# Optimization experiments

Hardware: AMD Instinct MI355X
Metric: run time of the kernel (lower is better)

## Reference

```python
import jax, jax.numpy as jnp
import numpy as np

B, S, H = 2, 4096, 2048
NH, HD = 16, 128
BLOCK = 256
EPS = 1e-5


def setup_inputs() -> dict:
    key = jax.random.key(0)
    ks = jax.random.split(key, 6)
    return {
        "hidden_states": jax.random.normal(ks[0], (B, S, H), jnp.float32),
        "attention_mask": jnp.ones((B, S), jnp.float32),
        "slope_rate": jax.random.uniform(ks[1], (NH,), jnp.float32),
        "w_qkv": jax.random.normal(ks[2], (H, 3 * NH * HD), jnp.float32) * 0.02,
        "w_gate": jax.random.normal(ks[3], (H, NH * HD), jnp.float32) * 0.02,
        "w_out": jax.random.normal(ks[4], (NH * HD, H), jnp.float32) * 0.02,
        "norm_weight": jnp.ones((NH * HD,), jnp.float32),
    }


def _lightning_attention(q, k, v, slope):
    # q,k,v: [b,h,n,d]; slope: [h] positive decay rates
    b, h, n, d = q.shape
    nc = n // BLOCK
    ar = jnp.arange(BLOCK, dtype=q.dtype) + 1.0  # 1..BLOCK
    s = slope[:, None, None]  # [h,1,1]
    q_decay = jnp.exp(-s * ar[None, :, None])             # [h,BLOCK,1]
    k_decay = jnp.exp(-s * (BLOCK - ar)[None, :, None])   # [h,BLOCK,1]
    idx = ar[:, None] - ar[None, :]                        # [BLOCK,BLOCK]
    mask = (idx >= 0).astype(q.dtype)
    # mask idx before exp so masked entries don't overflow (keeps grads finite)
    diag_decay = jnp.exp(-s * (idx * mask)[None]) * mask[None]  # [h,BLOCK,BLOCK]
    block_decay = jnp.exp(-slope * BLOCK)[None, :, None, None]  # [1,h,1,1]

    def to_chunks(x):
        return x.reshape(b, h, nc, BLOCK, d).transpose(2, 0, 1, 3, 4)

    qc, kc, vc = to_chunks(q), to_chunks(k), to_chunks(v)

    def step(kv, xs):
        qi, ki, vi = xs  # [b,h,BLOCK,d]
        # inter-chunk: decayed query against carried state kv [b,h,d,d]
        o_inter = jnp.einsum("bhmd,bhde->bhme", qi * q_decay, kv)
        # intra-chunk: causal decayed attention
        attn = jnp.einsum("bhmd,bhnd->bhmn", qi, ki) * diag_decay
        o = o_inter + jnp.einsum("bhmn,bhne->bhme", attn, vi)
        kv = block_decay * kv + jnp.einsum("bhnd,bhne->bhde", ki * k_decay, vi)
        return kv, o

    kv0 = jnp.zeros((b, h, d, d), q.dtype)
    _, o = jax.lax.scan(step, kv0, (qc, kc, vc))  # o: [nc,b,h,BLOCK,d]
    return o.transpose(1, 2, 0, 3, 4).reshape(b, h, n, d)


def reference(hidden_states, attention_mask, slope_rate, w_qkv, w_gate, w_out, norm_weight):
    b, n, _ = hidden_states.shape
    qkv = jax.nn.silu(hidden_states @ w_qkv)  # act on fused qkv
    q, k, v = jnp.split(qkv, 3, axis=-1)

    def heads(x):
        return x.reshape(b, n, NH, HD).transpose(0, 2, 1, 3)

    q, k, v = heads(q), heads(k), heads(v)
    v = v * attention_mask[:, None, :, None]  # zero padded tokens
    o = _lightning_attention(q, k, v, slope_rate)  # [b,h,n,d]
    o = o.transpose(0, 2, 1, 3).reshape(b, n, NH * HD)
    # RMSNorm over head_dim*num_heads
    var = jnp.mean(o * o, axis=-1, keepdims=True)
    o = o * jax.lax.rsqrt(var + EPS) * norm_weight
    # sigmoid output gate from raw hidden_states
    o = jax.nn.sigmoid(hidden_states @ w_gate) * o
    return o @ w_out
```

## Files before the change

### kernel.cpp

```cpp
#include <hip/hip_runtime.h>
#include <cstdint>

#define B_ 2
#define S_ 4096
#define H_ 2048
#define NH_ 16
#define HD_ 128
#define BLOCK_ 256
#define NC_ (S_/BLOCK_)
#define M_ (B_*S_)
#define EPS_ 1e-5f

typedef unsigned short ushort_t;
typedef unsigned short u16x4 __attribute__((ext_vector_type(4)));
typedef short frag_ab __attribute__((ext_vector_type(8)));
typedef float frag_cd __attribute__((ext_vector_type(4)));

static __device__ inline float bf2f(ushort_t u) {
    union { unsigned int i; float f; } x;
    x.i = ((unsigned int)u) << 16;
    return x.f;
}
static __device__ inline ushort_t f2bf(float f) {
    union { float f; unsigned int i; } x;
    x.f = f;
    unsigned int r = x.i + 0x7fffu + ((x.i >> 16) & 1u);
    return (ushort_t)(r >> 16);
}

static __device__ __forceinline__ void gload_lds16(const ushort_t* g, ushort_t* l) {
    __builtin_amdgcn_global_load_lds(
        (__attribute__((address_space(1))) void*)(uintptr_t)g,
        (__attribute__((address_space(3))) void*)l,
        16, 0, 0);
}

__global__ __launch_bounds__(256)
void cast_bf16_kernel(const float* __restrict__ in, ushort_t* __restrict__ out)
{
    int i = blockIdx.x * 256 + threadIdx.x;
    float4 v = reinterpret_cast<const float4*>(in)[i];
    u16x4 o = { f2bf(v.x), f2bf(v.y), f2bf(v.z), f2bf(v.w) };
    *reinterpret_cast<u16x4*>(&out[(size_t)i * 4]) = o;
}

__global__ __launch_bounds__(256)
void transpose_cast_kernel(const float* __restrict__ W, ushort_t* __restrict__ WT,
                           int K, int N)
{
    __shared__ float t[32][33];
    const int kb = blockIdx.y * 32, nb = blockIdx.x * 32;
    const int tx = threadIdx.x & 31, ty = threadIdx.x >> 5;
    #pragma unroll
    for (int i = 0; i < 4; ++i)
        t[ty + i * 8][tx] = W[(size_t)(kb + ty + i * 8) * N + nb + tx];
    __syncthreads();
    #pragma unroll
    for (int i = 0; i < 4; ++i)
        WT[(size_t)(nb + ty + i * 8) * K + kb + tx] = f2bf(t[tx][ty + i * 8]);
}

template<int MODE>
__global__ __launch_bounds__(256)
void gemm_mfma(const ushort_t* __restrict__ A, const ushort_t* __restrict__ BT,
               int M, int N, int K,
               float* __restrict__ Cf, ushort_t* __restrict__ Cb,
               ushort_t* __restrict__ qo, ushort_t* __restrict__ ko,
               ushort_t* __restrict__ kTo, ushort_t* __restrict__ vTo,
               const float* __restrict__ mask)
{
    __shared__ __align__(16) ushort_t As[128 * 32];
    __shared__ __align__(16) ushort_t Bs[128 * 32];
    const int tid  = threadIdx.x;
    const int lane = tid & 63, wid = tid >> 6;
    const int wr = wid >> 1, wc = wid & 1;
    const int l15 = lane & 15, l4 = lane >> 4;
    const int rowBase = blockIdx.y * 128, colBase = blockIdx.x * 128;

    const int srow = tid >> 2;
    const int sk   = (tid & 3) * 8;

    frag_cd acc[4][4];
    #pragma unroll
    for (int m = 0; m < 4; ++m)
        #pragma unroll
        for (int n = 0; n < 4; ++n) acc[m][n] = 0.f;

    for (int kt = 0; kt < K; kt += 32) {
        __syncthreads();
        #pragma unroll
        for (int j = 0; j < 2; ++j) {
            gload_lds16(A  + (size_t)(rowBase + j * 64 + srow) * K + kt + sk,
                        &As[j * 2048 + wid * 512]);
            gload_lds16(BT + (size_t)(colBase + j * 64 + srow) * K + kt + sk,
                        &Bs[j * 2048 + wid * 512]);
        }
        __syncthreads();

        frag_ab af[4], bf[4];
        #pragma unroll
        for (int m = 0; m < 4; ++m)
            af[m] = *reinterpret_cast<const frag_ab*>(&As[(wr * 64 + m * 16 + l15) * 32 + l4 * 8]);
        #pragma unroll
        for (int n = 0; n < 4; ++n)
            bf[n] = *reinterpret_cast<const frag_ab*>(&Bs[(wc * 64 + n * 16 + l15) * 32 + l4 * 8]);
        #pragma unroll
        for (int m = 0; m < 4; ++m)
            #pragma unroll
            for (int n = 0; n < 4; ++n)
                acc[m][n] = __builtin_amdgcn_mfma_f32_16x16x32_bf16(af[m], bf[n], acc[m][n], 0, 0, 0);
    }

    const int orow0 = rowBase + wr * 64;
    const int ocol0 = colBase + wc * 64;
    if (MODE == 0) {
        #pragma unroll
        for (int m = 0; m < 4; ++m)
            #pragma unroll
            for (int n = 0; n < 4; ++n)
                #pragma unroll
                for (int r = 0; r < 4; ++r) {
                    int row = orow0 + m * 16 + l4 * 4 + r;
                    int col = ocol0 + n * 16 + l15;
                    Cf[(size_t)row * N + col] = acc[m][n][r];
                }
    } else if (MODE == 1) {
        #pragma unroll
        for (int m = 0; m < 4; ++m)
            #pragma unroll
            for (int n = 0; n < 4; ++n)
                #pragma unroll
                for (int r = 0; r < 4; ++r) {
                    int row = orow0 + m * 16 + l4 * 4 + r;
                    int col = ocol0 + n * 16 + l15;
                    float x = acc[m][n][r];
                    Cb[(size_t)row * N + col] = f2bf(1.f / (1.f + __expf(-x)));
                }
    } else {
        const int which = colBase >> 11;
        const int h     = (colBase >> 7) & 15;
        #pragma unroll
        for (int m = 0; m < 4; ++m) {
            int row0 = orow0 + m * 16 + l4 * 4;
            int b = row0 >> 12, sr0 = row0 & 4095;
            int bh = b * NH_ + h;
            #pragma unroll
            for (int n = 0; n < 4; ++n) {
                int d = (ocol0 & 127) + n * 16 + l15;
                float sv[4];
                #pragma unroll
                for (int r = 0; r < 4; ++r) {
                    float x = acc[m][n][r];
                    sv[r] = x / (1.f + __expf(-x));
                }
                if (which == 0) {
                    #pragma unroll
                    for (int r = 0; r < 4; ++r)
                        qo[((size_t)bh * S_ + sr0 + r) * HD_ + d] = f2bf(sv[r]);
                } else if (which == 1) {
                    u16x4 pk;
                    #pragma unroll
                    for (int r = 0; r < 4; ++r) {
                        ushort_t u = f2bf(sv[r]);
                        ko[((size_t)bh * S_ + sr0 + r) * HD_ + d] = u;
                        pk[r] = u;
                    }
                    *reinterpret_cast<u16x4*>(&kTo[((size_t)bh * HD_ + d) * S_ + sr0]) = pk;
                } else {
                    u16x4 pk;
                    #pragma unroll
                    for (int r = 0; r < 4; ++r)
                        pk[r] = f2bf(sv[r] * mask[b * S_ + sr0 + r]);
                    *reinterpret_cast<u16x4*>(&vTo[((size_t)bh * HD_ + d) * S_ + sr0]) = pk;
                }
            }
        }
    }
}

__global__ __launch_bounds__(256)
void kv_chunk_mfma(const ushort_t* __restrict__ kT, const ushort_t* __restrict__ vT,
                   const float* __restrict__ slope, ushort_t* __restrict__ kvT)
{
    const int c = blockIdx.x, bh = blockIdx.y;
    const float s = slope[bh & 15];
    const int tid = threadIdx.x, lane = tid & 63, w = tid >> 6;
    const int l15 = lane & 15, l4 = lane >> 4;
    __shared__ float dec[BLOCK_];
    __shared__ __align__(16) ushort_t VTl[128 * 64];
    __shared__ __align__(16) ushort_t KTl[128 * 64];
    dec[tid] = __expf(-s * (float)(BLOCK_ - 1 - tid));

    frag_cd acc[2][8];
    #pragma unroll
    for (int mf = 0; mf < 2; ++mf)
        #pragma unroll
        for (int df = 0; df < 8; ++df) acc[mf][df] = 0.f;

    for (int nt = 0; nt < 4; ++nt) {
        __syncthreads();
        #pragma unroll
        for (int i = 0; i < 4; ++i) {
            int u = tid + i * 256;
            int row = u >> 3, slot = u & 7;
            size_t gsrc = ((size_t)bh * HD_ + row) * S_ + c * BLOCK_ + nt * 64 + slot * 8;
            frag_ab v8 = *reinterpret_cast<const frag_ab*>(vT + gsrc);
            *reinterpret_cast<frag_ab*>((char*)VTl + row * 128 + ((slot * 16) ^ ((row & 7) << 4))) = v8;
            frag_ab k8 = *reinterpret_cast<const frag_ab*>(kT + gsrc);
            frag_ab kd;
            #pragma unroll
            for (int j = 0; j < 8; ++j)
                kd[j] = (short)f2bf(bf2f((ushort_t)k8[j]) * dec[nt * 64 + slot * 8 + j]);
            *reinterpret_cast<frag_ab*>((char*)KTl + row * 128 + ((slot * 16) ^ ((row & 7) << 4))) = kd;
        }
        __syncthreads();
        #pragma unroll
        for (int ks = 0; ks < 2; ++ks) {
            frag_ab a[2];
            #pragma unroll
            for (int mf = 0; mf < 2; ++mf)
                a[mf] = *reinterpret_cast<const frag_ab*>(
                    (char*)VTl + (w * 32 + mf * 16 + l15) * 128 + ((ks * 64 + l4 * 16) ^ ((l15 & 7) << 4)));
            #pragma unroll
            for (int df = 0; df < 8; ++df) {
                frag_ab bk = *reinterpret_cast<const frag_ab*>(
                    (char*)KTl + (df * 16 + l15) * 128 + ((ks * 64 + l4 * 16) ^ ((l15 & 7) << 4)));
                acc[0][df] = __builtin_amdgcn_mfma_f32_16x16x32_bf16(a[0], bk, acc[0][df], 0, 0, 0);
                acc[1][df] = __builtin_amdgcn_mfma_f32_16x16x32_bf16(a[1], bk, acc[1][df], 0, 0, 0);
            }
        }
    }
    ushort_t* out = kvT + ((size_t)bh * NC_ + c) * 16384;
    #pragma unroll
    for (int mf = 0; mf < 2; ++mf)
        #pragma unroll
        for (int df = 0; df < 8; ++df)
            #pragma unroll
            for (int r = 0; r < 4; ++r) {
                int e = w * 32 + mf * 16 + l4 * 4 + r;
                int d = df * 16 + l15;
                out[e * 128 + d] = f2bf(acc[mf][df][r]);
            }
}

__global__ __launch_bounds__(256)
void kv_scan_kernel(const float* __restrict__ slope, const ushort_t* __restrict__ kvT,
                    ushort_t* __restrict__ sT)
{
    const int es = blockIdx.x, bh = blockIdx.y;
    const float s = slope[bh & 15];
    const float bd = __expf(-s * (float)BLOCK_);
    const int tid = threadIdx.x;
    float st[16];
    #pragma unroll
    for (int i = 0; i < 16; ++i) st[i] = 0.f;
    for (int c = 0; c < NC_; ++c) {
        const ushort_t* p = kvT + ((size_t)bh * NC_ + c) * 16384;
        ushort_t* qp = sT + ((size_t)bh * NC_ + c) * 16384;
        #pragma unroll
        for (int i = 0; i < 16; ++i) {
            int lin = tid + i * 256;
            int off = (lin >> 5) * 128 + es * 32 + (lin & 31);
            float x = bf2f(p[off]);
            qp[off] = f2bf(st[i]);
            st[i] = bd * st[i] + x;
        }
    }
}

__global__ __launch_bounds__(512)
void attn_mfma(const ushort_t* __restrict__ q, const ushort_t* __restrict__ k,
               const ushort_t* __restrict__ vT, const ushort_t* __restrict__ sT,
               const float* __restrict__ slope, float* __restrict__ o)
{
    const int c = blockIdx.x, bh = blockIdx.y;
    const int h = bh & 15, b = bh >> 4;
    const float s = slope[h];
    const int tid = threadIdx.x, lane = tid & 63, w = tid >> 6;
    const int l15 = lane & 15, l4 = lane >> 4;

    __shared__ __align__(16) ushort_t SH[16384];
    __shared__ __align__(16) ushort_t P[8][2048];

    frag_ab aq[2][4];
    #pragma unroll
    for (int mf = 0; mf < 2; ++mf)
        #pragma unroll
        for (int ks = 0; ks < 4; ++ks) {
            int row = c * BLOCK_ + w * 32 + mf * 16 + l15;
            aq[mf][ks] = *reinterpret_cast<const frag_ab*>(
                q + ((size_t)bh * S_ + row) * HD_ + ks * 32 + l4 * 8);
        }

    frag_cd oa[2][8];
    #pragma unroll
    for (int mf = 0; mf < 2; ++mf)
        #pragma unroll
        for (int ef = 0; ef < 8; ++ef) oa[mf][ef] = 0.f;

    const int wrow = w * 32;
    for (int nt = 0; nt < 4; ++nt) {
        __syncthreads();
        #pragma unroll
        for (int i = 0; i < 2; ++i) {
            int u = tid + i * 512;
            int n = u >> 4, slot = u & 15;
            frag_ab k8 = *reinterpret_cast<const frag_ab*>(
                k + ((size_t)bh * S_ + c * BLOCK_ + nt * 64 + n) * HD_ + slot * 8);
            *reinterpret_cast<frag_ab*>((char*)SH + n * 256 + ((slot * 16) ^ ((n & 7) << 4))) = k8;
        }
        #pragma unroll
        for (int i = 0; i < 2; ++i) {
            int u = tid + i * 512;
            int e = u >> 3, slot = u & 7;
            frag_ab v8 = *reinterpret_cast<const frag_ab*>(
                vT + ((size_t)bh * HD_ + e) * S_ + c * BLOCK_ + nt * 64 + slot * 8);
            *reinterpret_cast<frag_ab*>((char*)SH + 16384 + e * 128 + ((slot * 16) ^ ((e & 7) << 4))) = v8;
        }
        __syncthreads();
        if (nt * 64 > wrow + 31) continue;

        frag_cd pacc[2][4];
        #pragma unroll
        for (int mf = 0; mf < 2; ++mf)
            #pragma unroll
            for (int nf = 0; nf < 4; ++nf) pacc[mf][nf] = 0.f;
        #pragma unroll
        for (int ks = 0; ks < 4; ++ks)
            #pragma unroll
            for (int nf = 0; nf < 4; ++nf) {
                frag_ab bk = *reinterpret_cast<const frag_ab*>(
                    (char*)SH + (nf * 16 + l15) * 256 + ((ks * 64 + l4 * 16) ^ ((l15 & 7) << 4)));
                pacc[0][nf] = __builtin_amdgcn_mfma_f32_16x16x32_bf16(aq[0][ks], bk, pacc[0][nf], 0, 0, 0);
                pacc[1][nf] = __builtin_amdgcn_mfma_f32_16x16x32_bf16(aq[1][ks], bk, pacc[1][nf], 0, 0, 0);
            }
        #pragma unroll
        for (int mf = 0; mf < 2; ++mf)
            #pragma unroll
            for (int nf = 0; nf < 4; ++nf)
                #pragma unroll
                for (int r = 0; r < 4; ++r) {
                    int m = mf * 16 + l4 * 4 + r;
                    int mrow = wrow + m;
                    int ncol = nt * 64 + nf * 16 + l15;
                    float pv = 0.f;
                    if (mrow >= ncol) pv = pacc[mf][nf][r] * __expf(s * (float)(ncol - mrow));
                    *reinterpret_cast<ushort_t*>(
                        (char*)&P[w][0] + m * 128 + (((nf * 16 + l15) * 2) ^ ((m & 7) << 4))) = f2bf(pv);
                }
        __builtin_amdgcn_sched_barrier(0);
        #pragma unroll
        for (int ks = 0; ks < 2; ++ks) {
            frag_ab ap[2];
            #pragma unroll
            for (int mf = 0; mf < 2; ++mf)
                ap[mf] = *reinterpret_cast<const frag_ab*>(
                    (char*)&P[w][0] + (mf * 16 + l15) * 128 + ((ks * 64 + l4 * 16) ^ ((l15 & 7) << 4)));
            #pragma unroll
            for (int ef = 0; ef < 8; ++ef) {
                frag_ab bv = *reinterpret_cast<const frag_ab*>(
                    (char*)SH + 16384 + (ef * 16 + l15) * 128 + ((ks * 64 + l4 * 16) ^ ((l15 & 7) << 4)));
                oa[0][ef] = __builtin_amdgcn_mfma_f32_16x16x32_bf16(ap[0], bv, oa[0][ef], 0, 0, 0);
                oa[1][ef] = __builtin_amdgcn_mfma_f32_16x16x32_bf16(ap[1], bv, oa[1][ef], 0, 0, 0);
            }
        }
    }

    __syncthreads();
    #pragma unroll
    for (int i = 0; i < 4; ++i) {
        int u = tid + i * 512;
        int e = u >> 4, slot = u & 15;
        frag_ab s8 = *reinterpret_cast<const frag_ab*>(
            sT + ((size_t)(bh * NC_ + c)) * 16384 + e * 128 + slot * 8);
        *reinterpret_cast<frag_ab*>((char*)SH + e * 256 + ((slot * 16) ^ ((e & 7) << 4))) = s8;
    }
    __syncthreads();
    #pragma unroll
    for (int mf = 0; mf < 2; ++mf) {
        float qd = __expf(-s * (float)(wrow + mf * 16 + l15 + 1));
        #pragma unroll
        for (int ks = 0; ks < 4; ++ks) {
            frag_ab v = aq[mf][ks];
            #pragma unroll
            for (int j = 0; j < 8; ++j)
                v[j] = (short)f2bf(bf2f((ushort_t)v[j]) * qd);
            aq[mf][ks] = v;
        }
    }
    #pragma unroll
    for (int ks = 0; ks < 4; ++ks)
        #pragma unroll
        for (int ef = 0; ef < 8; ++ef) {
            frag_ab bs = *reinterpret_cast<const frag_ab*>(
                (char*)SH + (ef * 16 + l15) * 256 + ((ks * 64 + l4 * 16) ^ ((l15 & 7) << 4)));
            oa[0][ef] = __builtin_amdgcn_mfma_f32_16x16x32_bf16(aq[0][ks], bs, oa[0][ef], 0, 0, 0);
            oa[1][ef] = __builtin_amdgcn_mfma_f32_16x16x32_bf16(aq[1][ks], bs, oa[1][ef], 0, 0, 0);
        }
    #pragma unroll
    for (int mf = 0; mf < 2; ++mf)
        #pragma unroll
        for (int ef = 0; ef < 8; ++ef)
            #pragma unroll
            for (int r = 0; r < 4; ++r) {
                int row = c * BLOCK_ + wrow + mf * 16 + l4 * 4 + r;
                int col = h * HD_ + ef * 16 + l15;
                o[((size_t)(b * S_ + row)) * H_ + col] = oa[mf][ef][r];
            }
}

__global__ __launch_bounds__(256)
void norm_gate_kernel(const float* __restrict__ o, const ushort_t* __restrict__ gate,
                      const float* __restrict__ nw, ushort_t* __restrict__ on)
{
    const int row = blockIdx.x;
    const int tid = threadIdx.x;
    const float* orow = o + (size_t)row * H_;
    const ushort_t* grow = gate + (size_t)row * H_;
    ushort_t* onrow = on + (size_t)row * H_;
    float vals[8];
    float ss = 0.f;
    #pragma unroll
    for (int i = 0; i < 8; ++i) {
        vals[i] = orow[tid + i * 256];
        ss += vals[i] * vals[i];
    }
    __shared__ float red[256];
    red[tid] = ss;
    __syncthreads();
    #pragma unroll
    for (int st = 128; st > 0; st >>= 1) {
        if (tid < st) red[tid] += red[tid + st];
        __syncthreads();
    }
    float scale = rsqrtf(red[0] * (1.f / (float)H_) + EPS_);
    #pragma unroll
    for (int i = 0; i < 8; ++i) {
        int cidx = tid + i * 256;
        onrow[cidx] = f2bf(vals[i] * scale * nw[cidx] * bf2f(grow[cidx]));
    }
}

extern "C" void kernel_launch(void* const* d_in, const int* in_sizes, int n_in,
                              void* d_out, int out_size, void* d_ws, size_t ws_size,
                              hipStream_t stream)
{
    const float* hidden = (const float*)d_in[0];
    const float* mask   = (const float*)d_in[1];
    const float* slope  = (const float*)d_in[2];
    const float* w_qkv  = (const float*)d_in[3];
    const float* w_gate = (const float*)d_in[4];
    const float* w_out  = (const float*)d_in[5];
    const float* nw     = (const float*)d_in[6];

    const size_t MH = (size_t)M_ * H_;
    ushort_t* hid_bf  = (ushort_t*)d_ws;
    ushort_t* on_ws   = hid_bf;
    ushort_t* wqkvT   = hid_bf + MH;
    ushort_t* wgateT  = wqkvT + (size_t)6144 * 2048;
    ushort_t* kvT_ws  = wqkvT;
    ushort_t* sT_ws   = wqkvT + MH / 2;
    ushort_t* woutT   = wqkvT;
    ushort_t* q_ws    = hid_bf + 2 * MH;
    ushort_t* k_ws    = q_ws + MH;
    ushort_t* vT_ws   = k_ws + MH;
    ushort_t* gate_ws = vT_ws + MH;
    ushort_t* kT_ws   = (ushort_t*)d_out;
    float*    o_f32   = (float*)d_out;

    dim3 blk(256);
    cast_bf16_kernel<<<(MH / 4) / 256, blk, 0, stream>>>(hidden, hid_bf);
    transpose_cast_kernel<<<dim3(6144 / 32, 2048 / 32), blk, 0, stream>>>(w_qkv, wqkvT, 2048, 6144);
    transpose_cast_kernel<<<dim3(2048 / 32, 2048 / 32), blk, 0, stream>>>(w_gate, wgateT, 2048, 2048);
    gemm_mfma<2><<<dim3(6144 / 128, M_ / 128), blk, 0, stream>>>(
        hid_bf, wqkvT, M_, 6144, 2048, nullptr, nullptr, q_ws, k_ws, kT_ws, vT_ws, mask);
    gemm_mfma<1><<<dim3(2048 / 128, M_ / 128), blk, 0, stream>>>(
        hid_bf, wgateT, M_, 2048, 2048, nullptr, gate_ws, nullptr, nullptr, nullptr, nullptr, nullptr);
    kv_chunk_mfma<<<dim3(NC_, B_ * NH_), blk, 0, stream>>>(kT_ws, vT_ws, slope, kvT_ws);
    kv_scan_kernel<<<dim3(4, B_ * NH_), blk, 0, stream>>>(slope, kvT_ws, sT_ws);
    attn_mfma<<<dim3(NC_, B_ * NH_), dim3(512), 0, stream>>>(
        q_ws, k_ws, vT_ws, sT_ws, slope, o_f32);
    transpose_cast_kernel<<<dim3(2048 / 32, 2048 / 32), blk, 0, stream>>>(w_out, woutT, 2048, 2048);
    norm_gate_kernel<<<M_, blk, 0, stream>>>(o_f32, gate_ws, nw, on_ws);
    gemm_mfma<0><<<dim3(2048 / 128, M_ / 128), blk, 0, stream>>>(
        on_ws, woutT, M_, 2048, 2048, (float*)d_out, nullptr, nullptr, nullptr, nullptr, nullptr, nullptr);
}
```

Before: 655.3 us.

## Replace GEMMs with 256x256 double-buffered swizzled MFMA kernel and fuse gate GEMM

Replaces the 128x128 single-buffered GEMM with a 256x256-tile, 512-thread kernel. It double-buffers LDS with XOR-swizzled layout, staggers global-to-LDS loads between MFMA phases with explicit waitcnt and barriers, raises wave priority during MFMA, and remaps workgroups for L2 locality. The gate projection is fused into the QKV GEMM by treating w_qkv and w_gate as one contiguous 8192-column weight, with a sigmoid epilogue on the last column range. This is meant to raise MFMA utilisation and cut one launch, but it relies on the weight workspaces being adjacent and on hand-tuned wait counts being correct.

```diff
diff --git a/kernel.cpp b/kernel.cpp
--- a/kernel.cpp
+++ b/kernel.cpp
@@ -35,6 +35,12 @@
         16, 0, 0);
 }
 
+#define FENCE_ asm volatile("" ::: "memory")
+#define LGKM0_ asm volatile("s_waitcnt lgkmcnt(0)" ::: "memory")
+#define VMW2_  asm volatile("s_waitcnt vmcnt(2)" ::: "memory")
+#define VMW4_  asm volatile("s_waitcnt vmcnt(4)" ::: "memory")
+#define VMW0_  asm volatile("s_waitcnt vmcnt(0)" ::: "memory")
+
 __global__ __launch_bounds__(256)
 void cast_bf16_kernel(const float* __restrict__ in, ushort_t* __restrict__ out)
 {
@@ -61,117 +67,211 @@
 }
 
 template<int MODE>
-__global__ __launch_bounds__(256)
-void gemm_mfma(const ushort_t* __restrict__ A, const ushort_t* __restrict__ BT,
-               int M, int N, int K,
-               float* __restrict__ Cf, ushort_t* __restrict__ Cb,
-               ushort_t* __restrict__ qo, ushort_t* __restrict__ ko,
-               ushort_t* __restrict__ kTo, ushort_t* __restrict__ vTo,
-               const float* __restrict__ mask)
-{
-    __shared__ __align__(16) ushort_t As[128 * 32];
-    __shared__ __align__(16) ushort_t Bs[128 * 32];
+__global__ __launch_bounds__(512, 2)
+void gemm256(const ushort_t* __restrict__ A, const ushort_t* __restrict__ BT,
+             int M, int N, int K,
+             float* __restrict__ Cf,
+             ushort_t* __restrict__ qo, ushort_t* __restrict__ ko,
+             ushort_t* __restrict__ kTo, ushort_t* __restrict__ vTo,
+             ushort_t* __restrict__ gateo, const float* __restrict__ mask)
+{
+    __shared__ __align__(16) ushort_t LA[2][16384];
+    __shared__ __align__(16) ushort_t LB[2][16384];
+
     const int tid  = threadIdx.x;
     const int lane = tid & 63, wid = tid >> 6;
-    const int wr = wid >> 1, wc = wid & 1;
+    const int wm = wid >> 2, wn = wid & 3;
     const int l15 = lane & 15, l4 = lane >> 4;
-    const int rowBase = blockIdx.y * 128, colBase = blockIdx.x * 128;
-
-    const int srow = tid >> 2;
-    const int sk   = (tid & 3) * 8;
-
-    frag_cd acc[4][4];
-    #pragma unroll
-    for (int m = 0; m < 4; ++m)
+    const int trow = tid >> 3;
+    const int xk   = (tid & 7) ^ (trow & 7);
+
+    const int nwg = gridDim.x;
+    const int lin = blockIdx.x;
+    const int virt = (lin & 7) * (nwg >> 3) + (lin >> 3);
+    const int NBX = N >> 8;
+    const int by = virt / NBX, bx = virt - by * NBX;
+    const int rowBase = by * 256, colBase = bx * 256;
+
+    frag_cd acc[8][4];
+    #pragma unroll
+    for (int m = 0; m < 8; ++m)
         #pragma unroll
         for (int n = 0; n < 4; ++n) acc[m][n] = 0.f;
 
-    for (int kt = 0; kt < K; kt += 32) {
-        __syncthreads();
-        #pragma unroll
-        for (int j = 0; j < 2; ++j) {
-            gload_lds16(A  + (size_t)(rowBase + j * 64 + srow) * K + kt + sk,
-                        &As[j * 2048 + wid * 512]);
-            gload_lds16(BT + (size_t)(colBase + j * 64 + srow) * K + kt + sk,
-                        &Bs[j * 2048 + wid * 512]);
-        }
-        __syncthreads();
-
-        frag_ab af[4], bf[4];
-        #pragma unroll
-        for (int m = 0; m < 4; ++m)
-            af[m] = *reinterpret_cast<const frag_ab*>(&As[(wr * 64 + m * 16 + l15) * 32 + l4 * 8]);
-        #pragma unroll
-        for (int n = 0; n < 4; ++n)
-            bf[n] = *reinterpret_cast<const frag_ab*>(&Bs[(wc * 64 + n * 16 + l15) * 32 + l4 * 8]);
-        #pragma unroll
-        for (int m = 0; m < 4; ++m)
-            #pragma unroll
-            for (int n = 0; n < 4; ++n)
-                acc[m][n] = __builtin_amdgcn_mfma_f32_16x16x32_bf16(af[m], bf[n], acc[m][n], 0, 0, 0);
-    }
-
-    const int orow0 = rowBase + wr * 64;
-    const int ocol0 = colBase + wc * 64;
+    frag_ab fa[4][2];
+    frag_ab fb[2][2][2];
+
+    #define RDF(Lp, row_, sl_) \
+        (*reinterpret_cast<const frag_ab*>( \
+            reinterpret_cast<const char*>(Lp) + (row_) * 128 + ((((sl_) ^ ((row_) & 7)) & 7) << 4)))
+    #define STG(Gp, base_, i_, kt_, Lp) \
+        gload_lds16((Gp) + (size_t)((base_) + (i_) * 64 + trow) * K + (kt_) + xk * 8, \
+                    (Lp) + (i_) * 4096 + wid * 512)
+
+    const int NT = K >> 6;
+    int cur = 0;
+    STG(BT, colBase, 0, 0, LB[0]); STG(BT, colBase, 1, 0, LB[0]);
+    STG(BT, colBase, 2, 0, LB[0]); STG(BT, colBase, 3, 0, LB[0]);
+    STG(A,  rowBase, 0, 0, LA[0]); STG(A,  rowBase, 2, 0, LA[0]);
+    STG(A,  rowBase, 1, 0, LA[0]); STG(A,  rowBase, 3, 0, LA[0]);
+    VMW2_; FENCE_; __builtin_amdgcn_s_barrier();
+
+    for (int t = 0; t < NT; ++t) {
+        const ushort_t* Ab = LA[cur];
+        const ushort_t* Bb = LB[cur];
+        ushort_t* An = LA[cur ^ 1];
+        ushort_t* Bn = LB[cur ^ 1];
+        const int ktn = (t + 1) << 6;
+        const bool more = (t + 1) < NT;
+
+        #pragma unroll
+        for (int mi = 0; mi < 4; ++mi)
+            #pragma unroll
+            for (int ks = 0; ks < 2; ++ks)
+                fa[mi][ks] = RDF(Ab, wm * 128 + mi * 16 + l15, ks * 4 + l4);
+        #pragma unroll
+        for (int ni = 0; ni < 2; ++ni)
+            #pragma unroll
+            for (int ks = 0; ks < 2; ++ks)
+                fb[0][ni][ks] = RDF(Bb, wn * 64 + ni * 16 + l15, ks * 4 + l4);
+        if (more) { STG(BT, colBase, 0, ktn, Bn); STG(BT, colBase, 1, ktn, Bn); }
+        FENCE_; __builtin_amdgcn_s_barrier(); LGKM0_;
+        __builtin_amdgcn_sched_barrier(0);
+        __builtin_amdgcn_s_setprio(1);
+        #pragma unroll
+        for (int mi = 0; mi < 4; ++mi)
+            #pragma unroll
+            for (int ni = 0; ni < 2; ++ni)
+                #pragma unroll
+                for (int ks = 0; ks < 2; ++ks)
+                    acc[mi][ni] = __builtin_amdgcn_mfma_f32_16x16x32_bf16(
+                        fa[mi][ks], fb[0][ni][ks], acc[mi][ni], 0, 0, 0);
+        __builtin_amdgcn_s_setprio(0);
+        FENCE_; __builtin_amdgcn_s_barrier();
+
+        #pragma unroll
+        for (int ni = 0; ni < 2; ++ni)
+            #pragma unroll
+            for (int ks = 0; ks < 2; ++ks)
+                fb[1][ni][ks] = RDF(Bb, wn * 64 + 32 + ni * 16 + l15, ks * 4 + l4);
+        if (more) { STG(BT, colBase, 2, ktn, Bn); STG(BT, colBase, 3, ktn, Bn); VMW4_; }
+        else      { VMW0_; }
+        FENCE_; __builtin_amdgcn_s_barrier(); LGKM0_;
+        __builtin_amdgcn_sched_barrier(0);
+        __builtin_amdgcn_s_setprio(1);
+        #pragma unroll
+        for (int mi = 0; mi < 4; ++mi)
+            #pragma unroll
+            for (int ni = 0; ni < 2; ++ni)
+                #pragma unroll
+                for (int ks = 0; ks < 2; ++ks)
+                    acc[mi][2 + ni] = __builtin_amdgcn_mfma_f32_16x16x32_bf16(
+                        fa[mi][ks], fb[1][ni][ks], acc[mi][2 + ni], 0, 0, 0);
+        __builtin_amdgcn_s_setprio(0);
+        FENCE_; __builtin_amdgcn_s_barrier();
+
+        #pragma unroll
+        for (int mi = 0; mi < 4; ++mi)
+            #pragma unroll
+            for (int ks = 0; ks < 2; ++ks)
+                fa[mi][ks] = RDF(Ab, wm * 128 + 64 + mi * 16 + l15, ks * 4 + l4);
+        if (more) { STG(A, rowBase, 0, ktn, An); STG(A, rowBase, 2, ktn, An); }
+        FENCE_; __builtin_amdgcn_s_barrier(); LGKM0_;
+        __builtin_amdgcn_sched_barrier(0);
+        __builtin_amdgcn_s_setprio(1);
+        #pragma unroll
+        for (int mi = 0; mi < 4; ++mi)
+            #pragma unroll
+            for (int ni = 0; ni < 2; ++ni)
+                #pragma unroll
+                for (int ks = 0; ks < 2; ++ks)
+                    acc[4 + mi][ni] = __builtin_amdgcn_mfma_f32_16x16x32_bf16(
+                        fa[mi][ks], fb[0][ni][ks], acc[4 + mi][ni], 0, 0, 0);
+        __builtin_amdgcn_s_setprio(0);
+        FENCE_; __builtin_amdgcn_s_barrier();
+
+        if (more) { STG(A, rowBase, 1, ktn, An); STG(A, rowBase, 3, ktn, An); VMW2_; }
+        FENCE_; __builtin_amdgcn_s_barrier(); LGKM0_;
+        __builtin_amdgcn_sched_barrier(0);
+        __builtin_amdgcn_s_setprio(1);
+        #pragma unroll
+        for (int mi = 0; mi < 4; ++mi)
+            #pragma unroll
+            for (int ni = 0; ni < 2; ++ni)
+                #pragma unroll
+                for (int ks = 0; ks < 2; ++ks)
+                    acc[4 + mi][2 + ni] = __builtin_amdgcn_mfma_f32_16x16x32_bf16(
+                        fa[mi][ks], fb[1][ni][ks], acc[4 + mi][2 + ni], 0, 0, 0);
+        __builtin_amdgcn_s_setprio(0);
+        FENCE_; __builtin_amdgcn_s_barrier();
+
+        cur ^= 1;
+    }
+    #undef RDF
+    #undef STG
+
+    const int row0 = rowBase + wm * 128;
+    const int c0   = colBase + wn * 64;
     if (MODE == 0) {
         #pragma unroll
-        for (int m = 0; m < 4; ++m)
-            #pragma unroll
-            for (int n = 0; n < 4; ++n)
+        for (int m = 0; m < 8; ++m) {
+            int mr = (m >> 2) * 64 + (m & 3) * 16;
+            #pragma unroll
+            for (int n = 0; n < 4; ++n) {
+                int nc = (n >> 1) * 32 + (n & 1) * 16;
                 #pragma unroll
                 for (int r = 0; r < 4; ++r) {
-                    int row = orow0 + m * 16 + l4 * 4 + r;
-                    int col = ocol0 + n * 16 + l15;
+                    int row = row0 + mr + l4 * 4 + r;
+                    int col = c0 + nc + l15;
                     Cf[(size_t)row * N + col] = acc[m][n][r];
                 }
-    } else if (MODE == 1) {
-        #pragma unroll
-        for (int m = 0; m < 4; ++m)
-            #pragma unroll
-            for (int n = 0; n < 4; ++n)
-                #pragma unroll
-                for (int r = 0; r < 4; ++r) {
-                    int row = orow0 + m * 16 + l4 * 4 + r;
-                    int col = ocol0 + n * 16 + l15;
-                    float x = acc[m][n][r];
-                    Cb[(size_t)row * N + col] = f2bf(1.f / (1.f + __expf(-x)));
-                }
+            }
+        }
     } else {
-        const int which = colBase >> 11;
-        const int h     = (colBase >> 7) & 15;
-        #pragma unroll
-        for (int m = 0; m < 4; ++m) {
-            int row0 = orow0 + m * 16 + l4 * 4;
-            int b = row0 >> 12, sr0 = row0 & 4095;
-            int bh = b * NH_ + h;
+        const int which = c0 >> 11;
+        const int h     = (c0 >> 7) & 15;
+        const int d0    = c0 & 127;
+        const int b     = row0 >> 12;
+        const int bh    = b * NH_ + h;
+        #pragma unroll
+        for (int m = 0; m < 8; ++m) {
+            int mr = (m >> 2) * 64 + (m & 3) * 16;
+            int sr0 = (row0 & 4095) + mr + l4 * 4;
             #pragma unroll
             for (int n = 0; n < 4; ++n) {
-                int d = (ocol0 & 127) + n * 16 + l15;
-                float sv[4];
-                #pragma unroll
-                for (int r = 0; r < 4; ++r) {
-                    float x = acc[m][n][r];
-                    sv[r] = x / (1.f + __expf(-x));
-                }
-                if (which == 0) {
-                    #pragma unroll
-                    for (int r = 0; r < 4; ++r)
-                        qo[((size_t)bh * S_ + sr0 + r) * HD_ + d] = f2bf(sv[r]);
-                } else if (which == 1) {
-                    u16x4 pk;
-                    #pragma unroll
-                    for (int r = 0; r < 4; ++r) {
-                        ushort_t u = f2bf(sv[r]);
-                        ko[((size_t)bh * S_ + sr0 + r) * HD_ + d] = u;
-                        pk[r] = u;
+                int nc = (n >> 1) * 32 + (n & 1) * 16;
+                float x0 = acc[m][n][0], x1 = acc[m][n][1];
+                float x2 = acc[m][n][2], x3 = acc[m][n][3];
+                if (which == 3) {
+                    int col_g = (c0 - 6144) + nc + l15;
+                    ushort_t* gp = gateo + (size_t)(row0 + mr + l4 * 4) * H_ + col_g;
+                    gp[0]       = f2bf(1.f / (1.f + __expf(-x0)));
+                    gp[H_]      = f2bf(1.f / (1.f + __expf(-x1)));
+                    gp[2 * H_]  = f2bf(1.f / (1.f + __expf(-x2)));
+                    gp[3 * H_]  = f2bf(1.f / (1.f + __expf(-x3)));
+                } else {
+                    int d = d0 + nc + l15;
+                    float s0 = x0 / (1.f + __expf(-x0));
+                    float s1 = x1 / (1.f + __expf(-x1));
+                    float s2 = x2 / (1.f + __expf(-x2));
+                    float s3 = x3 / (1.f + __expf(-x3));
+                    if (which == 0) {
+                        ushort_t* qp = qo + ((size_t)bh * S_ + sr0) * HD_ + d;
+                        qp[0]        = f2bf(s0);
+                        qp[HD_]      = f2bf(s1);
+                        qp[2 * HD_]  = f2bf(s2);
+                        qp[3 * HD_]  = f2bf(s3);
+                    } else if (which == 1) {
+                        u16x4 pk = { f2bf(s0), f2bf(s1), f2bf(s2), f2bf(s3) };
+                        ushort_t* kp = ko + ((size_t)bh * S_ + sr0) * HD_ + d;
+                        kp[0] = pk[0]; kp[HD_] = pk[1]; kp[2 * HD_] = pk[2]; kp[3 * HD_] = pk[3];
+                        *reinterpret_cast<u16x4*>(&kTo[((size_t)bh * HD_ + d) * S_ + sr0]) = pk;
+                    } else {
+                        float mk0 = mask[b * S_ + sr0],     mk1 = mask[b * S_ + sr0 + 1];
+                        float mk2 = mask[b * S_ + sr0 + 2], mk3 = mask[b * S_ + sr0 + 3];
+                        u16x4 pk = { f2bf(s0 * mk0), f2bf(s1 * mk1), f2bf(s2 * mk2), f2bf(s3 * mk3) };
+                        *reinterpret_cast<u16x4*>(&vTo[((size_t)bh * HD_ + d) * S_ + sr0]) = pk;
                     }
-                    *reinterpret_cast<u16x4*>(&kTo[((size_t)bh * HD_ + d) * S_ + sr0]) = pk;
-                } else {
-                    u16x4 pk;
-                    #pragma unroll
-                    for (int r = 0; r < 4; ++r)
-                        pk[r] = f2bf(sv[r] * mask[b * S_ + sr0 + r]);
-                    *reinterpret_cast<u16x4*>(&vTo[((size_t)bh * HD_ + d) * S_ + sr0]) = pk;
                 }
             }
         }
@@ -472,16 +572,16 @@
     cast_bf16_kernel<<<(MH / 4) / 256, blk, 0, stream>>>(hidden, hid_bf);
     transpose_cast_kernel<<<dim3(6144 / 32, 2048 / 32), blk, 0, stream>>>(w_qkv, wqkvT, 2048, 6144);
     transpose_cast_kernel<<<dim3(2048 / 32, 2048 / 32), blk, 0, stream>>>(w_gate, wgateT, 2048, 2048);
-    gemm_mfma<2><<<dim3(6144 / 128, M_ / 128), blk, 0, stream>>>(
-        hid_bf, wqkvT, M_, 6144, 2048, nullptr, nullptr, q_ws, k_ws, kT_ws, vT_ws, mask);
-    gemm_mfma<1><<<dim3(2048 / 128, M_ / 128), blk, 0, stream>>>(
-        hid_bf, wgateT, M_, 2048, 2048, nullptr, gate_ws, nullptr, nullptr, nullptr, nullptr, nullptr);
+    gemm256<2><<<dim3((M_ / 256) * (8192 / 256)), dim3(512), 0, stream>>>(
+        hid_bf, wqkvT, M_, 8192, 2048,
+        nullptr, q_ws, k_ws, kT_ws, vT_ws, gate_ws, mask);
     kv_chunk_mfma<<<dim3(NC_, B_ * NH_), blk, 0, stream>>>(kT_ws, vT_ws, slope, kvT_ws);
     kv_scan_kernel<<<dim3(4, B_ * NH_), blk, 0, stream>>>(slope, kvT_ws, sT_ws);
     attn_mfma<<<dim3(NC_, B_ * NH_), dim3(512), 0, stream>>>(
         q_ws, k_ws, vT_ws, sT_ws, slope, o_f32);
     transpose_cast_kernel<<<dim3(2048 / 32, 2048 / 32), blk, 0, stream>>>(w_out, woutT, 2048, 2048);
     norm_gate_kernel<<<M_, blk, 0, stream>>>(o_f32, gate_ws, nw, on_ws);
-    gemm_mfma<0><<<dim3(2048 / 128, M_ / 128), blk, 0, stream>>>(
-        on_ws, woutT, M_, 2048, 2048, (float*)d_out, nullptr, nullptr, nullptr, nullptr, nullptr, nullptr);
-}
+    gemm256<0><<<dim3((M_ / 256) * (2048 / 256)), dim3(512), 0, stream>>>(
+        on_ws, woutT, M_, 2048, 2048,
+        (float*)d_out, nullptr, nullptr, nullptr, nullptr, nullptr, nullptr);
+}
```

New measurement: 561.9 us. 1.17x faster.
